# Kernel tuning notes

Measured on AMD Instinct MI355X. Metric: run time of the kernel, lower is better.

## Reference

```python
import jax, jax.numpy as jnp
import numpy as np

B, S, D, H, DH = 2, 4096, 768, 12, 64

def setup_inputs() -> dict:
    key = jax.random.key(0)
    kx, kq, kk, kv = jax.random.split(key, 4)
    x = jax.random.normal(kx, (B, S, D), dtype=jnp.float32)
    # per-head Q/K/V projection weights, stacked over heads: [H, d_in, d_out]
    Wq = jax.random.normal(kq, (H, D, DH), dtype=jnp.float32) * 0.02
    Wk = jax.random.normal(kk, (H, D, DH), dtype=jnp.float32) * 0.02
    Wv = jax.random.normal(kv, (H, D, DH), dtype=jnp.float32) * 0.02
    return {"x": x, "Wq": Wq, "Wk": Wk, "Wv": Wv}

def reference(x, Wq, Wk, Wv):
    b, s, _ = x.shape
    # per-head linear projections (qkv_bias=False), batched over heads
    q = jnp.einsum('bsd,hde->bhse', x, Wq)  # [B,H,S,DH]
    k = jnp.einsum('bsd,hde->bhse', x, Wk)
    v = jnp.einsum('bsd,hde->bhse', x, Wv)
    scale = 1.0 / jnp.sqrt(jnp.asarray(q.shape[-1], q.dtype))
    scores = jnp.einsum('bhqe,bhke->bhqk', q, k) * scale  # [B,H,S,S]
    causal_mask = jnp.triu(jnp.ones((s, s), dtype=bool), k=1)
    scores = jnp.where(causal_mask, -jnp.inf, scores)
    attn = jax.nn.softmax(scores, axis=-1)  # dropout p=0 -> identity
    ctx = jnp.einsum('bhqk,bhke->bhqe', attn, v)  # [B,H,S,DH]
    # concat heads on last dim (matches torch.cat of per-head outputs)
    return ctx.transpose(0, 2, 1, 3).reshape(b, s, -1)  # [B,S,H*DH]
```

## Files before the change

kernel.cpp:

```cpp
#include <hip/hip_runtime.h>
#include <hip/hip_bf16.h>
#include <stdint.h>

#define B_  2
#define S_  4096
#define D_  768
#define H_  12
#define DH_ 64
#define BS_ (B_*S_)

typedef __bf16 bf16x8 __attribute__((ext_vector_type(8)));
typedef short  svec8  __attribute__((ext_vector_type(8)));
typedef float  fvec4  __attribute__((ext_vector_type(4)));
typedef unsigned short ushort_t;

__device__ __forceinline__ ushort_t f2bf(float f){
    unsigned u = __builtin_bit_cast(unsigned, f);
    unsigned r = (u + 0x7fffu + ((u >> 16) & 1u)) >> 16;
    return (ushort_t)r;
}

__device__ __forceinline__ fvec4 mfma16(svec8 a, svec8 b, fvec4 c){
    return __builtin_amdgcn_mfma_f32_16x16x32_bf16(
        __builtin_bit_cast(bf16x8, a), __builtin_bit_cast(bf16x8, b), c, 0, 0, 0);
}

__global__ __launch_bounds__(256) void qkv_proj(
    const float* __restrict__ X,
    const float* __restrict__ Wq, const float* __restrict__ Wk, const float* __restrict__ Wv,
    ushort_t* __restrict__ Qb, ushort_t* __restrict__ Kb, ushort_t* __restrict__ Vg)
{
    const int m0 = blockIdx.x * 128;
    const int h  = blockIdx.y;
    const int wt = blockIdx.z;
    const float* W  = (wt == 0) ? Wq : (wt == 1) ? Wk : Wv;
    const float* Wh = W + (size_t)h * (D_ * DH_);
    const float oscale = (wt == 0) ? 0.18033688011112042f : 1.0f;

    __shared__ ushort_t smem[128 * 72 + 64 * 64];
    ushort_t* Xs  = smem;
    ushort_t* Wts = smem + 128 * 72;
    ushort_t* XsT = smem;

    const int tid  = threadIdx.x;
    const int w    = tid >> 6;
    const int lane = tid & 63;
    const int quad = lane >> 4;
    const int l15  = lane & 15;

    fvec4 acc[2][4];
    #pragma unroll
    for (int i = 0; i < 2; i++)
        #pragma unroll
        for (int j = 0; j < 4; j++) acc[i][j] = (fvec4){0.f, 0.f, 0.f, 0.f};

    for (int k0 = 0; k0 < D_; k0 += 64) {
        #pragma unroll
        for (int i = 0; i < 4; i++) {
            int v = tid + 256 * i;
            int r = v >> 3, c = (v & 7) * 8;
            const float* src = X + (size_t)(m0 + r) * D_ + k0 + c;
            float4 d0 = *(const float4*)(src);
            float4 d1 = *(const float4*)(src + 4);
            svec8 pk;
            pk[0] = (short)f2bf(d0.x); pk[1] = (short)f2bf(d0.y);
            pk[2] = (short)f2bf(d0.z); pk[3] = (short)f2bf(d0.w);
            pk[4] = (short)f2bf(d1.x); pk[5] = (short)f2bf(d1.y);
            pk[6] = (short)f2bf(d1.z); pk[7] = (short)f2bf(d1.w);
            *(svec8*)(Xs + r * 72 + c) = pk;
        }
        #pragma unroll
        for (int i = 0; i < 4; i++) {
            int v = tid + 256 * i;
            int k = v >> 4, t = v & 15;
            float4 d = *(const float4*)(Wh + (size_t)(k0 + k) * DH_ + t * 4);
            #pragma unroll
            for (int j = 0; j < 4; j++) {
                int n = t * 4 + j;
                int addr = n * 64 + ((((k >> 3) ^ (t & 7))) << 3) + (k & 7);
                Wts[addr] = f2bf(j == 0 ? d.x : j == 1 ? d.y : j == 2 ? d.z : d.w);
            }
        }
        __syncthreads();

        #pragma unroll
        for (int ks = 0; ks < 2; ks++) {
            svec8 a0 = *(const svec8*)(Xs + (32 * w + l15) * 72 + ks * 32 + quad * 8);
            svec8 a1 = *(const svec8*)(Xs + (32 * w + 16 + l15) * 72 + ks * 32 + quad * 8);
            #pragma unroll
            for (int ns = 0; ns < 4; ns++) {
                int n = ns * 16 + l15;
                int swz = (ks * 4 + quad) ^ ((n >> 2) & 7);
                svec8 b = *(const svec8*)(Wts + n * 64 + swz * 8);
                acc[0][ns] = mfma16(a0, b, acc[0][ns]);
                acc[1][ns] = mfma16(a1, b, acc[1][ns]);
            }
        }
        __syncthreads();
    }

    if (wt != 2) {
        ushort_t* Out = (wt == 0) ? Qb : Kb;
        #pragma unroll
        for (int ms = 0; ms < 2; ms++)
            #pragma unroll
            for (int ns = 0; ns < 4; ns++)
                #pragma unroll
                for (int r = 0; r < 4; r++) {
                    int row = m0 + 32 * w + ms * 16 + quad * 4 + r;
                    int col = h * DH_ + ns * 16 + l15;
                    Out[(size_t)row * D_ + col] = f2bf(acc[ms][ns][r] * oscale);
                }
    } else {
        #pragma unroll
        for (int ms = 0; ms < 2; ms++)
            #pragma unroll
            for (int ns = 0; ns < 4; ns++)
                #pragma unroll
                for (int r = 0; r < 4; r++) {
                    int sl = 32 * w + ms * 16 + quad * 4 + r;
                    int e  = ns * 16 + l15;
                    XsT[e * 136 + sl] = f2bf(acc[ms][ns][r]);
                }
        __syncthreads();
        #pragma unroll
        for (int i = 0; i < 4; i++) {
            int v = tid + 256 * i;
            int e = v >> 4, s0 = (v & 15) * 8;
            svec8 d = *(const svec8*)(XsT + e * 136 + s0);
            *(svec8*)(Vg + (size_t)(h * DH_ + e) * BS_ + m0 + s0) = d;
        }
    }
}

__global__ __launch_bounds__(256, 5) void attn(
    const ushort_t* __restrict__ Qb, const ushort_t* __restrict__ Kb,
    const ushort_t* __restrict__ Vg, float* __restrict__ Out)
{
    const int fid = blockIdx.x;
    const int qt  = (S_ / 64 - 1) - fid / (H_ * B_);
    const int r24 = fid % (H_ * B_);
    const int h   = r24 % H_;
    const int b   = r24 / H_;
    const int q0 = qt * 64;

    const int tid  = threadIdx.x;
    const int w    = tid >> 6;
    const int lane = tid & 63;
    const int quad = lane >> 4;
    const int l15  = lane & 15;

    __shared__ ushort_t Ks[64 * 72];
    __shared__ ushort_t Vt[64 * 72];

    const size_t hb = (size_t)b * S_ * D_ + (size_t)h * DH_;
    const ushort_t* Vh = Vg + (size_t)h * DH_ * BS_ + (size_t)b * S_;

    const int sr = tid >> 3;
    const int sc = (tid & 7) * 8;
    const int pr0 = (((sr      >> 2) & 1) << 5) | (((sr      >> 5) & 1) << 4) |
                    (((sr      >> 4) & 1) << 3) | (((sr      >> 3) & 1) << 2) | (sr & 3);
    const int sr1 = sr + 32;
    const int pr1 = (((sr1 >> 2) & 1) << 5) | (((sr1 >> 5) & 1) << 4) |
                    (((sr1 >> 4) & 1) << 3) | (((sr1 >> 3) & 1) << 2) | (sr1 & 3);

    svec8 aq[2];
    {
        const ushort_t* qrow = Qb + hb + (size_t)(q0 + 16 * w + l15) * D_;
        aq[0] = *(const svec8*)(qrow + quad * 8);
        aq[1] = *(const svec8*)(qrow + 32 + quad * 8);
    }

    float m_i = -INFINITY;
    float ls  = 0.f;
    fvec4 acc[4];
    #pragma unroll
    for (int n = 0; n < 4; n++) acc[n] = (fvec4){0.f, 0.f, 0.f, 0.f};

    svec8 kd[2], vd[2];
    #pragma unroll
    for (int i = 0; i < 2; i++) {
        int r = sr + 32 * i;
        kd[i] = *(const svec8*)(Kb + hb + (size_t)r * D_ + sc);
        vd[i] = *(const svec8*)(Vh + (size_t)r * BS_ + sc);
    }
    *(svec8*)(Ks + pr0 * 72 + sc) = kd[0];
    *(svec8*)(Ks + pr1 * 72 + sc) = kd[1];
    *(svec8*)(Vt + sr  * 72 + sc) = vd[0];
    *(svec8*)(Vt + sr1 * 72 + sc) = vd[1];

    for (int kt = 0; kt <= qt; ++kt) {
        __syncthreads();

        if (kt < qt) {
            #pragma unroll
            for (int i = 0; i < 2; i++) {
                int r = sr + 32 * i;
                kd[i] = *(const svec8*)(Kb + hb + (size_t)((kt + 1) * 64 + r) * D_ + sc);
                vd[i] = *(const svec8*)(Vh + (size_t)r * BS_ + (kt + 1) * 64 + sc);
            }
        }

        fvec4 st[4];
        #pragma unroll
        for (int n = 0; n < 4; n++) st[n] = (fvec4){0.f, 0.f, 0.f, 0.f};
        #pragma unroll
        for (int ks = 0; ks < 2; ks++)
            #pragma unroll
            for (int n = 0; n < 4; n++) {
                svec8 ka = *(const svec8*)(Ks + (n * 16 + l15) * 72 + ks * 32 + quad * 8);
                st[n] = mfma16(ka, aq[ks], st[n]);
            }

        if (kt == qt) {
            #pragma unroll
            for (int n = 0; n < 4; n++)
                #pragma unroll
                for (int r = 0; r < 4; r++) {
                    int key = (n & 1) * 32 + quad * 8 + (n >> 1) * 4 + r;
                    int row = 16 * w + l15;
                    if (key > row) st[n][r] = -INFINITY;
                }
        }

        float mx = fmaxf(fmaxf(fmaxf(st[0][0], st[0][1]), fmaxf(st[0][2], st[0][3])),
                         fmaxf(fmaxf(st[1][0], st[1][1]), fmaxf(st[1][2], st[1][3])));
        float mx2 = fmaxf(fmaxf(fmaxf(st[2][0], st[2][1]), fmaxf(st[2][2], st[2][3])),
                          fmaxf(fmaxf(st[3][0], st[3][1]), fmaxf(st[3][2], st[3][3])));
        mx = fmaxf(mx, mx2);
        mx = fmaxf(mx, __shfl_xor(mx, 16));
        mx = fmaxf(mx, __shfl_xor(mx, 32));
        float mn = fmaxf(m_i, mx);
        float alpha = exp2f(m_i - mn);
        m_i = mn;
        ls *= alpha;

        svec8 ap0, ap1;
        #pragma unroll
        for (int n = 0; n < 4; n++)
            #pragma unroll
            for (int r = 0; r < 4; r++) {
                float p = exp2f(st[n][r] - mn);
                ls += p;
                ushort_t pb = (ushort_t)(__builtin_bit_cast(unsigned, p) >> 16);
                if (n & 1) ap1[(n >> 1) * 4 + r] = (short)pb;
                else       ap0[(n >> 1) * 4 + r] = (short)pb;
            }

        float ar[4];
        #pragma unroll
        for (int r = 0; r < 4; r++)
            ar[r] = __shfl(alpha, quad * 16 + quad * 4 + r);
        #pragma unroll
        for (int n = 0; n < 4; n++)
            #pragma unroll
            for (int r = 0; r < 4; r++) acc[n][r] *= ar[r];

        #pragma unroll
        for (int ks = 0; ks < 2; ks++) {
            svec8 ap = ks ? ap1 : ap0;
            #pragma unroll
            for (int n = 0; n < 4; n++) {
                svec8 bv = *(const svec8*)(Vt + (n * 16 + l15) * 72 + ks * 32 + quad * 8);
                acc[n] = mfma16(ap, bv, acc[n]);
            }
        }

        __syncthreads();

        if (kt < qt) {
            *(svec8*)(Ks + pr0 * 72 + sc) = kd[0];
            *(svec8*)(Ks + pr1 * 72 + sc) = kd[1];
            *(svec8*)(Vt + sr  * 72 + sc) = vd[0];
            *(svec8*)(Vt + sr1 * 72 + sc) = vd[1];
        }
    }

    float lsum = ls;
    lsum += __shfl_xor(lsum, 16);
    lsum += __shfl_xor(lsum, 32);
    float li[4];
    #pragma unroll
    for (int r = 0; r < 4; r++)
        li[r] = __shfl(lsum, quad * 16 + quad * 4 + r);
    #pragma unroll
    for (int n = 0; n < 4; n++)
        #pragma unroll
        for (int r = 0; r < 4; r++) {
            int row = q0 + 16 * w + quad * 4 + r;
            int col = h * DH_ + n * 16 + l15;
            Out[((size_t)b * S_ + row) * D_ + col] = acc[n][r] / li[r];
        }
}

extern "C" void kernel_launch(void* const* d_in, const int* in_sizes, int n_in,
                              void* d_out, int out_size, void* d_ws, size_t ws_size,
                              hipStream_t stream)
{
    const float* X  = (const float*)d_in[0];
    const float* Wq = (const float*)d_in[1];
    const float* Wk = (const float*)d_in[2];
    const float* Wv = (const float*)d_in[3];

    ushort_t* Qb = (ushort_t*)d_ws;
    ushort_t* Kb = Qb + (size_t)BS_ * D_;
    ushort_t* Vg = Kb + (size_t)BS_ * D_;
    float* Out = (float*)d_out;

    qkv_proj<<<dim3(64, H_, 3), dim3(256), 0, stream>>>(X, Wq, Wk, Wv, Qb, Kb, Vg);
    attn<<<dim3((S_ / 64) * H_ * B_), dim3(256), 0, stream>>>(Qb, Kb, Vg, Out);
}
```

Before: 250.3 us.

## Fuse Q/K/V projections per block, skip redundant rescale, pack bf16 conversion

The projection kernel now computes Q, K and V in one block, so each X tile is loaded and converted to bf16 once instead of three times. The price is triple the weight shared memory and accumulator registers, plus a third as many blocks. The attention kernel skips the accumulator rescale when no lane's running max grows, converts P to bf16 with the packed v_cvt_pk_bf16_f32 instruction, and advances K/V pointers incrementally instead of recomputing addresses. The packed conversion rounds instead of truncating, which slightly changes numerics.

```diff
diff --git a/kernel.cpp b/kernel.cpp
--- a/kernel.cpp
+++ b/kernel.cpp
@@ -12,6 +12,7 @@
 typedef __bf16 bf16x8 __attribute__((ext_vector_type(8)));
 typedef short  svec8  __attribute__((ext_vector_type(8)));
 typedef float  fvec4  __attribute__((ext_vector_type(4)));
+typedef int    ivec4  __attribute__((ext_vector_type(4)));
 typedef unsigned short ushort_t;
 
 __device__ __forceinline__ ushort_t f2bf(float f){
@@ -20,24 +21,29 @@
     return (ushort_t)r;
 }
 
+__device__ __forceinline__ unsigned cvt_pk_bf16(float lo, float hi){
+    unsigned r;
+    asm("v_cvt_pk_bf16_f32 %0, %1, %2" : "=v"(r) : "v"(lo), "v"(hi));
+    return r;
+}
+
 __device__ __forceinline__ fvec4 mfma16(svec8 a, svec8 b, fvec4 c){
     return __builtin_amdgcn_mfma_f32_16x16x32_bf16(
         __builtin_bit_cast(bf16x8, a), __builtin_bit_cast(bf16x8, b), c, 0, 0, 0);
 }
 
-__global__ __launch_bounds__(256) void qkv_proj(
+__global__ __launch_bounds__(256, 3) void qkv_proj(
     const float* __restrict__ X,
     const float* __restrict__ Wq, const float* __restrict__ Wk, const float* __restrict__ Wv,
     ushort_t* __restrict__ Qb, ushort_t* __restrict__ Kb, ushort_t* __restrict__ Vg)
 {
     const int m0 = blockIdx.x * 128;
     const int h  = blockIdx.y;
-    const int wt = blockIdx.z;
-    const float* W  = (wt == 0) ? Wq : (wt == 1) ? Wk : Wv;
-    const float* Wh = W + (size_t)h * (D_ * DH_);
-    const float oscale = (wt == 0) ? 0.18033688011112042f : 1.0f;
-
-    __shared__ ushort_t smem[128 * 72 + 64 * 64];
+    const float* Whs[3] = { Wq + (size_t)h * (D_ * DH_),
+                            Wk + (size_t)h * (D_ * DH_),
+                            Wv + (size_t)h * (D_ * DH_) };
+
+    __shared__ ushort_t smem[128 * 72 + 3 * 64 * 64];
     ushort_t* Xs  = smem;
     ushort_t* Wts = smem + 128 * 72;
     ushort_t* XsT = smem;
@@ -48,11 +54,13 @@
     const int quad = lane >> 4;
     const int l15  = lane & 15;
 
-    fvec4 acc[2][4];
-    #pragma unroll
-    for (int i = 0; i < 2; i++)
-        #pragma unroll
-        for (int j = 0; j < 4; j++) acc[i][j] = (fvec4){0.f, 0.f, 0.f, 0.f};
+    fvec4 acc[3][2][4];
+    #pragma unroll
+    for (int wt = 0; wt < 3; wt++)
+        #pragma unroll
+        for (int i = 0; i < 2; i++)
+            #pragma unroll
+            for (int j = 0; j < 4; j++) acc[wt][i][j] = (fvec4){0.f, 0.f, 0.f, 0.f};
 
     for (int k0 = 0; k0 < D_; k0 += 64) {
         #pragma unroll
@@ -70,17 +78,19 @@
             *(svec8*)(Xs + r * 72 + c) = pk;
         }
         #pragma unroll
-        for (int i = 0; i < 4; i++) {
-            int v = tid + 256 * i;
-            int k = v >> 4, t = v & 15;
-            float4 d = *(const float4*)(Wh + (size_t)(k0 + k) * DH_ + t * 4);
-            #pragma unroll
-            for (int j = 0; j < 4; j++) {
-                int n = t * 4 + j;
-                int addr = n * 64 + ((((k >> 3) ^ (t & 7))) << 3) + (k & 7);
-                Wts[addr] = f2bf(j == 0 ? d.x : j == 1 ? d.y : j == 2 ? d.z : d.w);
-            }
-        }
+        for (int wt = 0; wt < 3; wt++)
+            #pragma unroll
+            for (int i = 0; i < 4; i++) {
+                int v = tid + 256 * i;
+                int k = v >> 4, t = v & 15;
+                float4 d = *(const float4*)(Whs[wt] + (size_t)(k0 + k) * DH_ + t * 4);
+                #pragma unroll
+                for (int j = 0; j < 4; j++) {
+                    int n = t * 4 + j;
+                    int addr = wt * 4096 + n * 64 + ((((k >> 3) ^ (t & 7))) << 3) + (k & 7);
+                    Wts[addr] = f2bf(j == 0 ? d.x : j == 1 ? d.y : j == 2 ? d.z : d.w);
+                }
+            }
         __syncthreads();
 
         #pragma unroll
@@ -88,48 +98,48 @@
             svec8 a0 = *(const svec8*)(Xs + (32 * w + l15) * 72 + ks * 32 + quad * 8);
             svec8 a1 = *(const svec8*)(Xs + (32 * w + 16 + l15) * 72 + ks * 32 + quad * 8);
             #pragma unroll
-            for (int ns = 0; ns < 4; ns++) {
-                int n = ns * 16 + l15;
-                int swz = (ks * 4 + quad) ^ ((n >> 2) & 7);
-                svec8 b = *(const svec8*)(Wts + n * 64 + swz * 8);
-                acc[0][ns] = mfma16(a0, b, acc[0][ns]);
-                acc[1][ns] = mfma16(a1, b, acc[1][ns]);
-            }
+            for (int wt = 0; wt < 3; wt++)
+                #pragma unroll
+                for (int ns = 0; ns < 4; ns++) {
+                    int n = ns * 16 + l15;
+                    int swz = (ks * 4 + quad) ^ ((n >> 2) & 7);
+                    svec8 b = *(const svec8*)(Wts + wt * 4096 + n * 64 + swz * 8);
+                    acc[wt][0][ns] = mfma16(a0, b, acc[wt][0][ns]);
+                    acc[wt][1][ns] = mfma16(a1, b, acc[wt][1][ns]);
+                }
         }
         __syncthreads();
     }
 
-    if (wt != 2) {
-        ushort_t* Out = (wt == 0) ? Qb : Kb;
-        #pragma unroll
-        for (int ms = 0; ms < 2; ms++)
-            #pragma unroll
-            for (int ns = 0; ns < 4; ns++)
-                #pragma unroll
-                for (int r = 0; r < 4; r++) {
-                    int row = m0 + 32 * w + ms * 16 + quad * 4 + r;
-                    int col = h * DH_ + ns * 16 + l15;
-                    Out[(size_t)row * D_ + col] = f2bf(acc[ms][ns][r] * oscale);
-                }
-    } else {
-        #pragma unroll
-        for (int ms = 0; ms < 2; ms++)
-            #pragma unroll
-            for (int ns = 0; ns < 4; ns++)
-                #pragma unroll
-                for (int r = 0; r < 4; r++) {
-                    int sl = 32 * w + ms * 16 + quad * 4 + r;
-                    int e  = ns * 16 + l15;
-                    XsT[e * 136 + sl] = f2bf(acc[ms][ns][r]);
-                }
-        __syncthreads();
-        #pragma unroll
-        for (int i = 0; i < 4; i++) {
-            int v = tid + 256 * i;
-            int e = v >> 4, s0 = (v & 15) * 8;
-            svec8 d = *(const svec8*)(XsT + e * 136 + s0);
-            *(svec8*)(Vg + (size_t)(h * DH_ + e) * BS_ + m0 + s0) = d;
-        }
+    const float qs = 0.18033688011112042f;
+    #pragma unroll
+    for (int ms = 0; ms < 2; ms++)
+        #pragma unroll
+        for (int ns = 0; ns < 4; ns++)
+            #pragma unroll
+            for (int r = 0; r < 4; r++) {
+                int row = m0 + 32 * w + ms * 16 + quad * 4 + r;
+                int col = h * DH_ + ns * 16 + l15;
+                Qb[(size_t)row * D_ + col] = f2bf(acc[0][ms][ns][r] * qs);
+                Kb[(size_t)row * D_ + col] = f2bf(acc[1][ms][ns][r]);
+            }
+    #pragma unroll
+    for (int ms = 0; ms < 2; ms++)
+        #pragma unroll
+        for (int ns = 0; ns < 4; ns++)
+            #pragma unroll
+            for (int r = 0; r < 4; r++) {
+                int sl = 32 * w + ms * 16 + quad * 4 + r;
+                int e  = ns * 16 + l15;
+                XsT[e * 136 + sl] = f2bf(acc[2][ms][ns][r]);
+            }
+    __syncthreads();
+    #pragma unroll
+    for (int i = 0; i < 4; i++) {
+        int v = tid + 256 * i;
+        int e = v >> 4, s0 = (v & 15) * 8;
+        svec8 d = *(const svec8*)(XsT + e * 136 + s0);
+        *(svec8*)(Vg + (size_t)(h * DH_ + e) * BS_ + m0 + s0) = d;
     }
 }
 
@@ -177,13 +187,16 @@
     #pragma unroll
     for (int n = 0; n < 4; n++) acc[n] = (fvec4){0.f, 0.f, 0.f, 0.f};
 
+    const ushort_t* kp = Kb + hb + (size_t)sr * D_ + sc;
+    const ushort_t* vp = Vh + (size_t)sr * BS_ + sc;
+
     svec8 kd[2], vd[2];
-    #pragma unroll
-    for (int i = 0; i < 2; i++) {
-        int r = sr + 32 * i;
-        kd[i] = *(const svec8*)(Kb + hb + (size_t)r * D_ + sc);
-        vd[i] = *(const svec8*)(Vh + (size_t)r * BS_ + sc);
-    }
+    kd[0] = *(const svec8*)(kp);
+    kd[1] = *(const svec8*)(kp + (size_t)32 * D_);
+    vd[0] = *(const svec8*)(vp);
+    vd[1] = *(const svec8*)(vp + (size_t)32 * BS_);
+    kp += (size_t)64 * D_;
+    vp += 64;
     *(svec8*)(Ks + pr0 * 72 + sc) = kd[0];
     *(svec8*)(Ks + pr1 * 72 + sc) = kd[1];
     *(svec8*)(Vt + sr  * 72 + sc) = vd[0];
@@ -193,12 +206,12 @@
         __syncthreads();
 
         if (kt < qt) {
-            #pragma unroll
-            for (int i = 0; i < 2; i++) {
-                int r = sr + 32 * i;
-                kd[i] = *(const svec8*)(Kb + hb + (size_t)((kt + 1) * 64 + r) * D_ + sc);
-                vd[i] = *(const svec8*)(Vh + (size_t)r * BS_ + (kt + 1) * 64 + sc);
-            }
+            kd[0] = *(const svec8*)(kp);
+            kd[1] = *(const svec8*)(kp + (size_t)32 * D_);
+            vd[0] = *(const svec8*)(vp);
+            vd[1] = *(const svec8*)(vp + (size_t)32 * BS_);
+            kp += (size_t)64 * D_;
+            vp += 64;
         }
 
         fvec4 st[4];
@@ -223,38 +236,52 @@
                 }
         }
 
-        float mx = fmaxf(fmaxf(fmaxf(st[0][0], st[0][1]), fmaxf(st[0][2], st[0][3])),
-                         fmaxf(fmaxf(st[1][0], st[1][1]), fmaxf(st[1][2], st[1][3])));
-        float mx2 = fmaxf(fmaxf(fmaxf(st[2][0], st[2][1]), fmaxf(st[2][2], st[2][3])),
-                          fmaxf(fmaxf(st[3][0], st[3][1]), fmaxf(st[3][2], st[3][3])));
-        mx = fmaxf(mx, mx2);
+        float mxa = fmaxf(fmaxf(st[0][0], st[0][1]), st[0][2]);
+        mxa = fmaxf(fmaxf(mxa, st[0][3]), st[1][0]);
+        mxa = fmaxf(fmaxf(mxa, st[1][1]), st[1][2]);
+        mxa = fmaxf(mxa, st[1][3]);
+        float mxb = fmaxf(fmaxf(st[2][0], st[2][1]), st[2][2]);
+        mxb = fmaxf(fmaxf(mxb, st[2][3]), st[3][0]);
+        mxb = fmaxf(fmaxf(mxb, st[3][1]), st[3][2]);
+        mxb = fmaxf(mxb, st[3][3]);
+        float mx = fmaxf(mxa, mxb);
         mx = fmaxf(mx, __shfl_xor(mx, 16));
         mx = fmaxf(mx, __shfl_xor(mx, 32));
-        float mn = fmaxf(m_i, mx);
-        float alpha = exp2f(m_i - mn);
-        m_i = mn;
-        ls *= alpha;
-
-        svec8 ap0, ap1;
-        #pragma unroll
-        for (int n = 0; n < 4; n++)
-            #pragma unroll
-            for (int r = 0; r < 4; r++) {
-                float p = exp2f(st[n][r] - mn);
-                ls += p;
-                ushort_t pb = (ushort_t)(__builtin_bit_cast(unsigned, p) >> 16);
-                if (n & 1) ap1[(n >> 1) * 4 + r] = (short)pb;
-                else       ap0[(n >> 1) * 4 + r] = (short)pb;
-            }
-
-        float ar[4];
-        #pragma unroll
-        for (int r = 0; r < 4; r++)
-            ar[r] = __shfl(alpha, quad * 16 + quad * 4 + r);
-        #pragma unroll
-        for (int n = 0; n < 4; n++)
-            #pragma unroll
-            for (int r = 0; r < 4; r++) acc[n][r] *= ar[r];
+
+        if (__any(mx > m_i)) {
+            float mn = fmaxf(m_i, mx);
+            float alpha = exp2f(m_i - mn);
+            m_i = mn;
+            ls *= alpha;
+            float ar[4];
+            #pragma unroll
+            for (int r = 0; r < 4; r++)
+                ar[r] = __shfl(alpha, quad * 16 + quad * 4 + r);
+            #pragma unroll
+            for (int n = 0; n < 4; n++)
+                #pragma unroll
+                for (int r = 0; r < 4; r++) acc[n][r] *= ar[r];
+        }
+
+        ivec4 ai0, ai1;
+        float psum[4];
+        #pragma unroll
+        for (int n = 0; n < 4; n++) {
+            float p0 = exp2f(st[n][0] - m_i);
+            float p1 = exp2f(st[n][1] - m_i);
+            float p2 = exp2f(st[n][2] - m_i);
+            float p3 = exp2f(st[n][3] - m_i);
+            psum[n] = (p0 + p1) + (p2 + p3);
+            unsigned d0 = cvt_pk_bf16(p0, p1);
+            unsigned d1 = cvt_pk_bf16(p2, p3);
+            if (n == 0)      { ai0[0] = (int)d0; ai0[1] = (int)d1; }
+            else if (n == 1) { ai1[0] = (int)d0; ai1[1] = (int)d1; }
+            else if (n == 2) { ai0[2] = (int)d0; ai0[3] = (int)d1; }
+            else             { ai1[2] = (int)d0; ai1[3] = (int)d1; }
+        }
+        ls += (psum[0] + psum[2]) + (psum[1] + psum[3]);
+        svec8 ap0 = __builtin_bit_cast(svec8, ai0);
+        svec8 ap1 = __builtin_bit_cast(svec8, ai1);
 
         #pragma unroll
         for (int ks = 0; ks < 2; ks++) {
@@ -307,6 +334,6 @@
     ushort_t* Vg = Kb + (size_t)BS_ * D_;
     float* Out = (float*)d_out;
 
-    qkv_proj<<<dim3(64, H_, 3), dim3(256), 0, stream>>>(X, Wq, Wk, Wv, Qb, Kb, Vg);
+    qkv_proj<<<dim3(64, H_), dim3(256), 0, stream>>>(X, Wq, Wk, Wv, Qb, Kb, Vg);
     attn<<<dim3((S_ / 64) * H_ * B_), dim3(256), 0, stream>>>(Qb, Kb, Vg, Out);
 }
```

Result: slower. 262.8 us (+5.0%).
